# Kernel optimization log

Hardware: AMD Instinct MI355X
Metric: run time of the kernel (lower is better)

The kernel has to match this reference:

```python
import jax, jax.numpy as jnp
import numpy as np
import math

D_MODEL = 1024
N_HEADS = 16
HEAD_DIM = 64


def setup_inputs() -> dict:
    key = jax.random.key(0)
    k_x, k_q, k_k, k_v, k_o = jax.random.split(key, 5)
    lecun = jax.nn.initializers.lecun_normal()
    return {
        "x": jax.random.normal(k_x, (4, 2048, D_MODEL), dtype=jnp.float32),
        "W_q": lecun(k_q, (N_HEADS, D_MODEL, HEAD_DIM), jnp.float32),
        "W_k": lecun(k_k, (N_HEADS, D_MODEL, HEAD_DIM), jnp.float32),
        "W_v": lecun(k_v, (N_HEADS, D_MODEL, HEAD_DIM), jnp.float32),
        "W_o": lecun(k_o, (D_MODEL, D_MODEL), jnp.float32),
    }


def reference(x, W_q, W_k, W_v, W_o):
    # x: [b, l, e]; W_{q,k,v}: [h, e, d]; W_o: [e, e]
    q = jnp.einsum('ble,hed->bhld', x, W_q)
    k = jnp.einsum('ble,hed->bhld', x, W_k)
    v = jnp.einsum('ble,hed->bhld', x, W_v)
    scores = jnp.einsum('bhld,bhsd->bhls', q, k) / math.sqrt(HEAD_DIM)
    attn = jax.nn.softmax(scores, axis=-1)
    av = jnp.einsum('bhls,bhsd->bhld', attn, v)  # [b, h, l, d]
    b, h, l, d = av.shape
    concat = jnp.transpose(av, (0, 2, 1, 3)).reshape(b, l, h * d)
    out = jnp.einsum('ble,eo->blo', concat, W_o)
    return jnp.asarray(out, dtype=jnp.float32)
```

## Files before the change

### kernel.cpp

```cpp
#include <hip/hip_runtime.h>

#define BATCH 4
#define LSEQ  2048
#define DM    1024
#define NH    16
#define HD    64
#define NTOK  (BATCH * LSEQ)

typedef _Float16 f16x8 __attribute__((ext_vector_type(8)));
typedef _Float16 f16x4 __attribute__((ext_vector_type(4)));
typedef __fp16   hf16x2 __attribute__((ext_vector_type(2)));
typedef float    f32x4 __attribute__((ext_vector_type(4)));
typedef float    f32x16 __attribute__((ext_vector_type(16)));

typedef __attribute__((address_space(1))) const unsigned int GU32;
typedef __attribute__((address_space(3))) unsigned int LU32;

__device__ __forceinline__ void gload_lds16(const _Float16* g, _Float16* l)
{
    __builtin_amdgcn_global_load_lds(
        (GU32*)(unsigned long long)g,
        (LU32*)(unsigned int)(unsigned long long)l, 16, 0, 0);
}


__global__ __launch_bounds__(256) void prep_kernel(
    const float* __restrict__ x,
    const float* __restrict__ Wq, const float* __restrict__ Wk,
    const float* __restrict__ Wv, const float* __restrict__ Wo,
    _Float16* __restrict__ xh, _Float16* __restrict__ WtA,
    _Float16* __restrict__ Wot)
{
    const int bid = blockIdx.x;
    const int t = threadIdx.x;

    if (bid < 8192) {
        int i = bid * 256 + t;
        float4 v = ((const float4*)x)[i];
        f16x4 h;
        h[0] = (_Float16)v.x; h[1] = (_Float16)v.y; h[2] = (_Float16)v.z; h[3] = (_Float16)v.w;
        ((f16x4*)xh)[i] = h;
        return;
    }

    __shared__ float Ls[64][65];

    if (bid < 8960) {
        const int idx = bid - 8192;
        const int z = idx >> 4;
        const int which = z >> 4, h = z & 15;
        const float* __restrict__ src =
            ((which == 0) ? Wq : (which == 1) ? Wk : Wv) + (size_t)h * DM * HD;
        _Float16* __restrict__ d = WtA + (size_t)z * DM * HD;
        const int e0 = (idx & 15) * 64;
        #pragma unroll
        for (int j = 0; j < 4; ++j) {
            int cidx = t + j * 256;
            int row = cidx >> 4, col4 = (cidx & 15) * 4;
            float4 v = *(const float4*)&src[(size_t)(e0 + row) * HD + col4];
            Ls[row][col4] = v.x; Ls[row][col4+1] = v.y; Ls[row][col4+2] = v.z; Ls[row][col4+3] = v.w;
        }
        __syncthreads();
        const int dd = t & 63, sc = t >> 6;
        alignas(16) _Float16 tmp[16];
        #pragma unroll
        for (int i = 0; i < 16; ++i) tmp[i] = (_Float16)Ls[sc * 16 + i][dd];
        *(f16x8*)&d[(size_t)dd * DM + e0 + sc * 16]     = *(f16x8*)&tmp[0];
        *(f16x8*)&d[(size_t)dd * DM + e0 + sc * 16 + 8] = *(f16x8*)&tmp[8];
        return;
    }

    {
        const int idx = bid - 8960;
        const int d0 = (idx & 15) * 64, e0 = (idx >> 4) * 64;
        #pragma unroll
        for (int j = 0; j < 4; ++j) {
            int cidx = t + j * 256;
            int row = cidx >> 4, col4 = (cidx & 15) * 4;
            float4 v = *(const float4*)&Wo[(size_t)(e0 + row) * DM + d0 + col4];
            Ls[row][col4] = v.x; Ls[row][col4+1] = v.y; Ls[row][col4+2] = v.z; Ls[row][col4+3] = v.w;
        }
        __syncthreads();
        const int dd = t & 63, sc = t >> 6;
        alignas(16) _Float16 tmp[16];
        #pragma unroll
        for (int i = 0; i < 16; ++i) tmp[i] = (_Float16)Ls[sc * 16 + i][dd];
        *(f16x8*)&Wot[(size_t)(d0 + dd) * DM + e0 + sc * 16]     = *(f16x8*)&tmp[0];
        *(f16x8*)&Wot[(size_t)(d0 + dd) * DM + e0 + sc * 16 + 8] = *(f16x8*)&tmp[8];
    }
}

template<int MODE>
__global__ __launch_bounds__(256) void gemm_kernel(
    const _Float16* __restrict__ A, const _Float16* __restrict__ B,
    float* __restrict__ out32,
    _Float16* __restrict__ qo, _Float16* __restrict__ ko, _Float16* __restrict__ vto)
{
    const int n0 = blockIdx.x * 128, m0 = blockIdx.y * 128;
    __shared__ _Float16 As[128 * 64];
    __shared__ _Float16 Bs[128 * 64];
    const int t = threadIdx.x;
    const int lane = t & 63, w = t >> 6;
    const int quad = lane >> 4, c = lane & 15;
    const int wm = (w & 1) * 64, wn = (w >> 1) * 64;
    const int srow = lane >> 3;
    const int scol8 = ((lane & 7) ^ (lane >> 3)) * 8;

    const int colsw = (quad ^ (c & 7)) * 8;
    const _Float16* Ap0 = &As[(wm + c) * 64 + colsw];
    const _Float16* Ap1 = &As[(wm + c) * 64 + (colsw ^ 32)];
    const _Float16* Bp0 = &Bs[(wn + c) * 64 + colsw];
    const _Float16* Bp1 = &Bs[(wn + c) * 64 + (colsw ^ 32)];

    f32x4 acc[4][4];
    #pragma unroll
    for (int i = 0; i < 4; ++i)
        #pragma unroll
        for (int j = 0; j < 4; ++j) acc[i][j] = {0.f, 0.f, 0.f, 0.f};

    for (int e0 = 0; e0 < DM; e0 += 64) {
        __syncthreads();
        #pragma unroll
        for (int j = 0; j < 4; ++j) {
            int ch = w * 4 + j;
            gload_lds16(A + (size_t)(m0 + ch * 8 + srow) * DM + e0 + scol8, As + ch * 512);
            gload_lds16(B + (size_t)(n0 + ch * 8 + srow) * DM + e0 + scol8, Bs + ch * 512);
        }
        __syncthreads();
        #pragma unroll
        for (int kc = 0; kc < 2; ++kc) {
            const _Float16* Ap = kc ? Ap1 : Ap0;
            const _Float16* Bp = kc ? Bp1 : Bp0;
            f16x8 af[4], bf[4];
            #pragma unroll
            for (int mt = 0; mt < 4; ++mt) af[mt] = *(const f16x8*)(Ap + mt * 1024);
            #pragma unroll
            for (int nt = 0; nt < 4; ++nt) bf[nt] = *(const f16x8*)(Bp + nt * 1024);
            #pragma unroll
            for (int mt = 0; mt < 4; ++mt)
                #pragma unroll
                for (int nt = 0; nt < 4; ++nt)
                    acc[mt][nt] = __builtin_amdgcn_mfma_f32_16x16x32_f16(af[mt], bf[nt], acc[mt][nt], 0, 0, 0);
        }
    }

    if (MODE == 0) {
        #pragma unroll
        for (int mt = 0; mt < 4; ++mt)
            #pragma unroll
            for (int nt = 0; nt < 4; ++nt)
                #pragma unroll
                for (int r = 0; r < 4; ++r) {
                    int row = m0 + wm + mt * 16 + quad * 4 + r;
                    int col = n0 + wn + nt * 16 + c;
                    out32[(size_t)row * DM + col] = acc[mt][nt][r];
                }
    } else {
        const int mi = (n0 + wn) >> 6;
        const int which = mi >> 4, hh = mi & 15;
        if (which == 2) {
            #pragma unroll
            for (int mt = 0; mt < 4; ++mt) {
                int tokb = m0 + wm + mt * 16;
                int btok = tokb >> 11;
                int lt   = tokb & (LSEQ - 1);
                int tau  = lt >> 6, sstep = (lt >> 4) & 3;
                int hlw  = quad & 1, jb = 4 * (quad >> 1);
                size_t bhbase = (size_t)(btok * NH + hh) * (32 * 8 * 512);
                #pragma unroll
                for (int nt = 0; nt < 4; ++nt) {
                    int d = nt * 16 + c;
                    int m2 = d & 31, dblk = d >> 5;
                    f16x4 pk;
                    pk[0] = (_Float16)acc[mt][nt][0];
                    pk[1] = (_Float16)acc[mt][nt][1];
                    pk[2] = (_Float16)acc[mt][nt][2];
                    pk[3] = (_Float16)acc[mt][nt][3];
                    size_t off = bhbase
                               + ((size_t)(tau * 8 + dblk * 4 + sstep) * 64 + hlw * 32 + m2) * 8 + jb;
                    *(f16x4*)&vto[off] = pk;
                }
            }
        } else {
            _Float16* dst = (which == 0) ? qo : ko;
            const float vs = (which == 0) ? 0.18033688011112042f : 1.0f;
            #pragma unroll
            for (int mt = 0; mt < 4; ++mt)
                #pragma unroll
                for (int nt = 0; nt < 4; ++nt)
                    #pragma unroll
                    for (int r = 0; r < 4; ++r) {
                        int tok = m0 + wm + mt * 16 + quad * 4 + r;
                        int b = tok >> 11, l = tok & (LSEQ - 1);
                        int d = nt * 16 + c;
                        dst[((size_t)(b * NH + hh) * LSEQ + l) * HD + d] = (_Float16)(acc[mt][nt][r] * vs);
                    }
        }
    }
}

__global__ __launch_bounds__(256, 4) void attn_kernel(
    const _Float16* __restrict__ Qg, const _Float16* __restrict__ Kg,
    const _Float16* __restrict__ Vtg, _Float16* __restrict__ concat)
{
    const int bh = blockIdx.x;
    const int q0 = blockIdx.y * 128;
    const int b = bh >> 4, head = bh & (NH - 1);
    __shared__ _Float16 Ks[2][64 * 64];
    const int t = threadIdx.x;
    const int lane = t & 63, w = t >> 6;
    const int m = lane & 31, hl = lane >> 5;
    const int srow = lane >> 3;
    const int scol8 = ((lane & 7) ^ (lane >> 3)) * 8;

    f16x8 qf[4];
    #pragma unroll
    for (int kstep = 0; kstep < 4; ++kstep)
        qf[kstep] = *(const f16x8*)&Qg[((size_t)bh * LSEQ + q0 + w * 32 + m) * HD + kstep * 16 + hl * 8];

    f32x16 o[2];
    #pragma unroll
    for (int i = 0; i < 16; ++i) { o[0][i] = 0.f; o[1][i] = 0.f; }
    float lp = 0.f;
    const hf16x2 ones2 = {(__fp16)1.0f, (__fp16)1.0f};

    auto stage = [&](int bi, int s0n) {
        #pragma unroll
        for (int j = 0; j < 2; ++j) {
            int ch = w * 2 + j;
            gload_lds16(Kg + ((size_t)bh * LSEQ + s0n + ch * 8 + srow) * HD + scol8, &Ks[bi][ch * 512]);
        }
    };

    const _Float16* Vbase = Vtg + (size_t)bh * (32 * 8 * 512) + (size_t)lane * 8;
    f16x8 vf[8];
    auto loadV = [&](int tile) {
        const _Float16* p = Vbase + (size_t)tile * 4096;
        #pragma unroll
        for (int q = 0; q < 8; ++q)
            vf[q] = *(const f16x8*)(p + q * 512);
    };

    constexpr int NT = LSEQ / 64;
    stage(0, 0);
    loadV(0);
    int cur = 0;

    for (int tt = 0; tt < NT; ++tt) {
        asm volatile("s_waitcnt vmcnt(8)" ::: "memory");
        __builtin_amdgcn_s_barrier();
        __builtin_amdgcn_sched_barrier(0);

        if (tt + 1 < NT) stage(cur ^ 1, (tt + 1) * 64);

        const _Float16* Kb = &Ks[cur][0];

        f16x8 pf[4];
        #pragma unroll
        for (int sblk = 0; sblk < 2; ++sblk) {
            const int rr = sblk * 32 + m;
            const int rx = rr & 7;
            const _Float16* Krow = Kb + rr * 64;
            f32x16 sT;
            #pragma unroll
            for (int i = 0; i < 16; ++i) sT[i] = 0.f;
            __builtin_amdgcn_s_setprio(1);
            #pragma unroll
            for (int kstep = 0; kstep < 4; ++kstep) {
                f16x8 kf = *(const f16x8*)(Krow + (((kstep * 2 + hl) ^ rx) * 8));
                sT = __builtin_amdgcn_mfma_f32_32x32x16_f16(kf, qf[kstep], sT, 0, 0, 0);
            }
            __builtin_amdgcn_s_setprio(0);
            union { unsigned int u[4]; f16x8 v; } P0, P1;
            #pragma unroll
            for (int q = 0; q < 8; ++q) {
                float e0 = __builtin_amdgcn_exp2f(sT[2 * q]);
                float e1 = __builtin_amdgcn_exp2f(sT[2 * q + 1]);
                union { hf16x2 h; unsigned int u; } uu;
                uu.h = __builtin_amdgcn_cvt_pkrtz(e0, e1);
                lp = __builtin_amdgcn_fdot2(uu.h, ones2, lp, false);
                if (q < 4) P0.u[q] = uu.u; else P1.u[q - 4] = uu.u;
            }
            pf[sblk * 2 + 0] = P0.v;
            pf[sblk * 2 + 1] = P1.v;
        }

        __builtin_amdgcn_s_setprio(1);
        #pragma unroll
        for (int dblk = 0; dblk < 2; ++dblk)
            #pragma unroll
            for (int sstep = 0; sstep < 4; ++sstep)
                o[dblk] = __builtin_amdgcn_mfma_f32_32x32x16_f16(pf[sstep], vf[dblk * 4 + sstep], o[dblk], 0, 0, 0);
        __builtin_amdgcn_s_setprio(0);

        if (tt + 1 < NT) loadV(tt + 1);

        asm volatile("s_waitcnt lgkmcnt(0)" ::: "memory");
        __builtin_amdgcn_sched_barrier(0);
        cur ^= 1;
    }

    lp += __shfl_xor(lp, 32);

    #pragma unroll
    for (int rg = 0; rg < 16; ++rg) {
        const int mrow = (rg & 3) + 8 * (rg >> 2) + 4 * hl;
        const float inv = 1.f / __shfl(lp, mrow);
        const int row = q0 + w * 32 + mrow;
        #pragma unroll
        for (int dblk = 0; dblk < 2; ++dblk)
            concat[((size_t)b * LSEQ + row) * DM + head * HD + dblk * 32 + m] =
                (_Float16)(o[dblk][rg] * inv);
    }
}

extern "C" void kernel_launch(void* const* d_in, const int* in_sizes, int n_in,
                              void* d_out, int out_size, void* d_ws, size_t ws_size,
                              hipStream_t stream)
{
    (void)in_sizes; (void)n_in; (void)out_size; (void)ws_size;

    const float* x  = (const float*)d_in[0];
    const float* Wq = (const float*)d_in[1];
    const float* Wk = (const float*)d_in[2];
    const float* Wv = (const float*)d_in[3];
    const float* Wo = (const float*)d_in[4];
    float* out = (float*)d_out;

    const size_t XE = (size_t)NTOK * DM;
    const size_t WQKV = (size_t)3 * NH * HD * DM;
    _Float16* xh  = (_Float16*)d_ws;
    _Float16* WtA = xh + XE;
    _Float16* Wot = WtA + WQKV;
    _Float16* q   = Wot + (size_t)DM * DM;
    _Float16* k   = q + XE;
    _Float16* vt  = k + XE;
    _Float16* cc  = vt + XE;

    prep_kernel<<<9216, 256, 0, stream>>>(x, Wq, Wk, Wv, Wo, xh, WtA, Wot);

    gemm_kernel<1><<<dim3(24, 64), 256, 0, stream>>>(xh, WtA, nullptr, q, k, vt);
    attn_kernel<<<dim3(64, LSEQ / 128), 256, 0, stream>>>(q, k, vt, cc);
    gemm_kernel<0><<<dim3(8, 64), 256, 0, stream>>>(cc, Wot, out, nullptr, nullptr, nullptr);
}
```

Baseline: 271.3 us.

## Add dedicated QKV projection GEMM with 256x192 tiles and double-buffered LDS

```diff
diff --git a/kernel.cpp b/kernel.cpp
--- a/kernel.cpp
+++ b/kernel.cpp
@@ -22,7 +22,6 @@
         (GU32*)(unsigned long long)g,
         (LU32*)(unsigned int)(unsigned long long)l, 16, 0, 0);
 }
-
 
 __global__ __launch_bounds__(256) void prep_kernel(
     const float* __restrict__ x,
@@ -90,11 +89,123 @@
     }
 }
 
+__global__ __launch_bounds__(512, 2) void gemm1_kernel(
+    const _Float16* __restrict__ A, const _Float16* __restrict__ Bg,
+    _Float16* __restrict__ qo, _Float16* __restrict__ ko, _Float16* __restrict__ vto)
+{
+    const int bid = blockIdx.x;
+    const int swz = (bid & 7) * 64 + (bid >> 3);
+    const int m0 = (swz & 31) * 256;
+    const int n0 = (swz >> 5) * 192;
+
+    __shared__ _Float16 As[2][256 * 32];
+    __shared__ _Float16 Bs[2][192 * 32];
+
+    const int t = threadIdx.x;
+    const int lane = t & 63, w = t >> 6;
+    const int quad = lane >> 4, c = lane & 15;
+    const int wm = (w & 1) * 128, wn = (w >> 1) * 48;
+    const int srow4 = lane >> 2;
+    const int sc8 = ((lane & 3) ^ (srow4 & 3)) * 8;
+    const int colsw4 = (quad ^ (c & 3)) * 8;
+
+    f32x4 acc[8][3];
+    #pragma unroll
+    for (int i = 0; i < 8; ++i)
+        #pragma unroll
+        for (int j = 0; j < 3; ++j) acc[i][j] = {0.f, 0.f, 0.f, 0.f};
+
+    auto stage = [&](int bi, int e0) {
+        if (w < 4) {
+            #pragma unroll
+            for (int j = 0; j < 4; ++j) {
+                int ch = w * 4 + j;
+                gload_lds16(A + (size_t)(m0 + ch * 16 + srow4) * DM + e0 + sc8,
+                            &As[bi][ch * 512]);
+            }
+        } else {
+            #pragma unroll
+            for (int j = 0; j < 3; ++j) {
+                int ch = (w - 4) * 3 + j;
+                gload_lds16(Bg + (size_t)(n0 + ch * 16 + srow4) * DM + e0 + sc8,
+                            &Bs[bi][ch * 512]);
+            }
+        }
+    };
+
+    stage(0, 0);
+    for (int T = 0; T < 32; ++T) {
+        const int bi = T & 1;
+        asm volatile("s_waitcnt vmcnt(0)" ::: "memory");
+        __builtin_amdgcn_s_barrier();
+        __builtin_amdgcn_sched_barrier(0);
+        if (T < 31) stage(bi ^ 1, (T + 1) * 32);
+
+        const _Float16* Ap = &As[bi][(wm + c) * 32 + colsw4];
+        const _Float16* Bp = &Bs[bi][(wn + c) * 32 + colsw4];
+        f16x8 af[8], bf[3];
+        #pragma unroll
+        for (int mt = 0; mt < 8; ++mt) af[mt] = *(const f16x8*)(Ap + mt * 512);
+        #pragma unroll
+        for (int nt = 0; nt < 3; ++nt) bf[nt] = *(const f16x8*)(Bp + nt * 512);
+        asm volatile("s_waitcnt lgkmcnt(0)" ::: "memory");
+        __builtin_amdgcn_sched_barrier(0);
+
+        __builtin_amdgcn_s_setprio(1);
+        #pragma unroll
+        for (int mt = 0; mt < 8; ++mt)
+            #pragma unroll
+            for (int nt = 0; nt < 3; ++nt)
+                acc[mt][nt] = __builtin_amdgcn_mfma_f32_16x16x32_f16(af[mt], bf[nt], acc[mt][nt], 0, 0, 0);
+        __builtin_amdgcn_s_setprio(0);
+    }
+
+    #pragma unroll
+    for (int nt = 0; nt < 3; ++nt) {
+        const int colb = n0 + wn + nt * 16;
+        const int g = colb >> 6;
+        const int which = g >> 4, hh = g & 15;
+        const int dlo = colb & 63;
+        if (which == 2) {
+            #pragma unroll
+            for (int mt = 0; mt < 8; ++mt) {
+                int tokb = m0 + wm + mt * 16;
+                int btok = tokb >> 11;
+                int lt   = tokb & (LSEQ - 1);
+                int tau  = lt >> 6, sstep = (lt >> 4) & 3;
+                int hlw  = quad & 1, jb = 4 * (quad >> 1);
+                size_t bhbase = (size_t)(btok * NH + hh) * (32 * 8 * 512);
+                int d = dlo + c;
+                int m2 = d & 31, dblk = d >> 5;
+                f16x4 pk;
+                pk[0] = (_Float16)acc[mt][nt][0];
+                pk[1] = (_Float16)acc[mt][nt][1];
+                pk[2] = (_Float16)acc[mt][nt][2];
+                pk[3] = (_Float16)acc[mt][nt][3];
+                size_t off = bhbase
+                           + ((size_t)(tau * 8 + dblk * 4 + sstep) * 64 + hlw * 32 + m2) * 8 + jb;
+                *(f16x4*)&vto[off] = pk;
+            }
+        } else {
+            _Float16* dst = (which == 0) ? qo : ko;
+            const float vs = (which == 0) ? 0.18033688011112042f : 1.0f;
+            #pragma unroll
+            for (int mt = 0; mt < 8; ++mt)
+                #pragma unroll
+                for (int r = 0; r < 4; ++r) {
+                    int tok = m0 + wm + mt * 16 + quad * 4 + r;
+                    int b = tok >> 11, l = tok & (LSEQ - 1);
+                    int d = dlo + c;
+                    dst[((size_t)(b * NH + hh) * LSEQ + l) * HD + d] = (_Float16)(acc[mt][nt][r] * vs);
+                }
+        }
+    }
+}
+
 template<int MODE>
 __global__ __launch_bounds__(256) void gemm_kernel(
     const _Float16* __restrict__ A, const _Float16* __restrict__ B,
-    float* __restrict__ out32,
-    _Float16* __restrict__ qo, _Float16* __restrict__ ko, _Float16* __restrict__ vto)
+    float* __restrict__ out32)
 {
     const int n0 = blockIdx.x * 128, m0 = blockIdx.y * 128;
     __shared__ _Float16 As[128 * 64];
@@ -144,59 +255,16 @@
         }
     }
 
-    if (MODE == 0) {
-        #pragma unroll
-        for (int mt = 0; mt < 4; ++mt)
-            #pragma unroll
-            for (int nt = 0; nt < 4; ++nt)
-                #pragma unroll
-                for (int r = 0; r < 4; ++r) {
-                    int row = m0 + wm + mt * 16 + quad * 4 + r;
-                    int col = n0 + wn + nt * 16 + c;
-                    out32[(size_t)row * DM + col] = acc[mt][nt][r];
-                }
-    } else {
-        const int mi = (n0 + wn) >> 6;
-        const int which = mi >> 4, hh = mi & 15;
-        if (which == 2) {
-            #pragma unroll
-            for (int mt = 0; mt < 4; ++mt) {
-                int tokb = m0 + wm + mt * 16;
-                int btok = tokb >> 11;
-                int lt   = tokb & (LSEQ - 1);
-                int tau  = lt >> 6, sstep = (lt >> 4) & 3;
-                int hlw  = quad & 1, jb = 4 * (quad >> 1);
-                size_t bhbase = (size_t)(btok * NH + hh) * (32 * 8 * 512);
-                #pragma unroll
-                for (int nt = 0; nt < 4; ++nt) {
-                    int d = nt * 16 + c;
-                    int m2 = d & 31, dblk = d >> 5;
-                    f16x4 pk;
-                    pk[0] = (_Float16)acc[mt][nt][0];
-                    pk[1] = (_Float16)acc[mt][nt][1];
-                    pk[2] = (_Float16)acc[mt][nt][2];
-                    pk[3] = (_Float16)acc[mt][nt][3];
-                    size_t off = bhbase
-                               + ((size_t)(tau * 8 + dblk * 4 + sstep) * 64 + hlw * 32 + m2) * 8 + jb;
-                    *(f16x4*)&vto[off] = pk;
-                }
-            }
-        } else {
-            _Float16* dst = (which == 0) ? qo : ko;
-            const float vs = (which == 0) ? 0.18033688011112042f : 1.0f;
-            #pragma unroll
-            for (int mt = 0; mt < 4; ++mt)
-                #pragma unroll
-                for (int nt = 0; nt < 4; ++nt)
-                    #pragma unroll
-                    for (int r = 0; r < 4; ++r) {
-                        int tok = m0 + wm + mt * 16 + quad * 4 + r;
-                        int b = tok >> 11, l = tok & (LSEQ - 1);
-                        int d = nt * 16 + c;
-                        dst[((size_t)(b * NH + hh) * LSEQ + l) * HD + d] = (_Float16)(acc[mt][nt][r] * vs);
-                    }
-        }
-    }
+    #pragma unroll
+    for (int mt = 0; mt < 4; ++mt)
+        #pragma unroll
+        for (int nt = 0; nt < 4; ++nt)
+            #pragma unroll
+            for (int r = 0; r < 4; ++r) {
+                int row = m0 + wm + mt * 16 + quad * 4 + r;
+                int col = n0 + wn + nt * 16 + c;
+                out32[(size_t)row * DM + col] = acc[mt][nt][r];
+            }
 }
 
 __global__ __launch_bounds__(256, 4) void attn_kernel(
@@ -339,7 +407,7 @@
 
     prep_kernel<<<9216, 256, 0, stream>>>(x, Wq, Wk, Wv, Wo, xh, WtA, Wot);
 
-    gemm_kernel<1><<<dim3(24, 64), 256, 0, stream>>>(xh, WtA, nullptr, q, k, vt);
+    gemm1_kernel<<<512, 512, 0, stream>>>(xh, WtA, q, k, vt);
     attn_kernel<<<dim3(64, LSEQ / 128), 256, 0, stream>>>(q, k, vt, cc);
-    gemm_kernel<0><<<dim3(8, 64), 256, 0, stream>>>(cc, Wot, out, nullptr, nullptr, nullptr);
-}
+    gemm_kernel<0><<<dim3(8, 64), 256, 0, stream>>>(cc, Wot, out);
+}
```

Measured after the change: 288.0 us. 6.2% more time.
